# Kernel optimization log

Hardware: AMD Instinct MI355X
Metric: run time of the kernel (lower is better)

The kernel has to match this reference:

```python
import jax, jax.numpy as jnp
import numpy as np

HIDDEN = 4096
NUM_HEADS = 32
NUM_KV_HEADS = 8
HEAD_DIM = HIDDEN // NUM_HEADS  # 128
ROPE_THETA = 500000.0
WORLD_SIZE = 4  # number of ring blocks (simulated single-device)


def setup_inputs() -> dict:
    key = jax.random.key(0)
    ks = jax.random.split(key, 5)
    B, S = 1, 2048
    wscale = HIDDEN ** -0.5  # keep activations O(1)
    return {
        "hidden_states": jax.random.normal(ks[0], (B, S, HIDDEN), jnp.float32),
        "position_ids": jnp.broadcast_to(jnp.arange(S, dtype=jnp.int32), (B, S)),
        "q_proj": jax.random.normal(ks[1], (NUM_HEADS * HEAD_DIM, HIDDEN), jnp.float32) * wscale,
        "k_proj": jax.random.normal(ks[2], (NUM_KV_HEADS * HEAD_DIM, HIDDEN), jnp.float32) * wscale,
        "v_proj": jax.random.normal(ks[3], (NUM_KV_HEADS * HEAD_DIM, HIDDEN), jnp.float32) * wscale,
        "o_proj": jax.random.normal(ks[4], (HIDDEN, NUM_HEADS * HEAD_DIM), jnp.float32) * wscale,
    }


def _rope_cos_sin(position_ids):
    # LlamaRotaryEmbedding: inv_freq over even dims, emb = cat(freqs, freqs)
    inv_freq = 1.0 / (ROPE_THETA ** (jnp.arange(0, HEAD_DIM, 2, dtype=jnp.float32) / HEAD_DIM))
    freqs = position_ids.astype(jnp.float32)[..., None] * inv_freq  # [B,S,HD/2]
    emb = jnp.concatenate([freqs, freqs], axis=-1)                  # [B,S,HD]
    return jnp.cos(emb), jnp.sin(emb)


def _rotate_half(x):
    x1, x2 = jnp.split(x, 2, axis=-1)
    return jnp.concatenate([-x2, x1], axis=-1)


def _attention_forward(hidden_states, q_proj, k_proj, v_proj, o_proj, position_ids):
    B, S, _ = hidden_states.shape
    # projections (no bias), layout [B, S, H, D] as in the source (view before RoPE)
    q = (hidden_states @ q_proj.T).reshape(B, S, NUM_HEADS, HEAD_DIM)
    k = (hidden_states @ k_proj.T).reshape(B, S, NUM_KV_HEADS, HEAD_DIM)
    v = (hidden_states @ v_proj.T).reshape(B, S, NUM_KV_HEADS, HEAD_DIM)

    cos, sin = _rope_cos_sin(position_ids)        # [B,S,HD]
    c, s = cos[:, :, None, :], sin[:, :, None, :]  # unsqueeze_dim=2
    q = q * c + _rotate_half(q) * s
    k = k * c + _rotate_half(k) * s

    # GQA: expand KV heads to match query heads
    groups = NUM_HEADS // NUM_KV_HEADS
    k = jnp.repeat(k, groups, axis=2)  # [B,S,NH,HD]
    v = jnp.repeat(v, groups, axis=2)

    sm_scale = HEAD_DIM ** -0.5
    blk = S // WORLD_SIZE

    # ring: per-KV-block partial attention (non-causal, as no mask is passed) + LSE
    outs, lses = [], []
    for w in range(WORLD_SIZE):
        kb = k[:, w * blk:(w + 1) * blk]
        vb = v[:, w * blk:(w + 1) * blk]
        scores = jnp.einsum('bqhd,bkhd->bhqk', q, kb) * sm_scale  # [B,NH,S,blk]
        m = jnp.max(scores, axis=-1, keepdims=True)
        p = jnp.exp(scores - m)
        l = jnp.sum(p, axis=-1, keepdims=True)
        outs.append(jnp.einsum('bhqk,bkhd->bqhd', p / l, vb))      # normalized partial out
        lses.append((m + jnp.log(l))[..., 0])                      # [B,NH,S]

    # merge_attentions: weight each block by exp(lse_b - logsumexp(lse))
    lse_all = jnp.stack(lses, axis=0)                 # [W,B,NH,S]
    wgt = jax.nn.softmax(lse_all, axis=0)
    attn = sum(outs[w] * jnp.transpose(wgt[w], (0, 2, 1))[..., None]
               for w in range(WORLD_SIZE))            # [B,S,NH,HD]

    attn = attn.reshape(B, S, NUM_HEADS * HEAD_DIM)
    return attn @ o_proj.T


def reference(hidden_states, position_ids, q_proj, k_proj, v_proj, o_proj):
    return _attention_forward(hidden_states, q_proj, k_proj, v_proj, o_proj, position_ids)
```

## Files before the change

### kernel.cpp

```cpp
#include <hip/hip_runtime.h>
#include <stdint.h>
#include <cmath>

typedef unsigned short u16;
typedef unsigned int u32;
typedef __attribute__((ext_vector_type(8))) __bf16 bf16x8;
typedef __attribute__((ext_vector_type(4))) float f32x4;

#define HIDDEN 4096
#define NH 32
#define NKV 8
#define HD 128
#define S_LEN 2048

__device__ __forceinline__ u16 f2bf(float f) {
    u32 x = __float_as_uint(f);
    x += 0x7fff + ((x >> 16) & 1);
    return (u16)(x >> 16);
}
__device__ __forceinline__ float bf2f(u16 u) {
    return __uint_as_float(((u32)u) << 16);
}
__device__ __forceinline__ float fexp2(float x) {
#if __has_builtin(__builtin_amdgcn_exp2f)
    return __builtin_amdgcn_exp2f(x);
#else
    return __expf(x * 0.6931471805599453f);
#endif
}

template <int N>
__device__ __forceinline__ float dpp_ror(float v) {
    int i = __builtin_amdgcn_update_dpp(0, __float_as_int(v),
                                        0x120 + N, 0xf, 0xf, true);
    return __int_as_float(i);
}
__device__ __forceinline__ float row_max16(float x) {
    x = fmaxf(x, dpp_ror<1>(x));
    x = fmaxf(x, dpp_ror<2>(x));
    x = fmaxf(x, dpp_ror<4>(x));
    x = fmaxf(x, dpp_ror<8>(x));
    return x;
}
__device__ __forceinline__ float row_sum16(float x) {
    x += dpp_ror<1>(x);
    x += dpp_ror<2>(x);
    x += dpp_ror<4>(x);
    x += dpp_ror<8>(x);
    return x;
}

typedef __attribute__((address_space(1))) const void gv_t;
typedef __attribute__((address_space(3))) void lv_t;
__device__ __forceinline__ void async16(const u16* g, u16* s) {
    __builtin_amdgcn_global_load_lds((gv_t*)g, (lv_t*)s, 16, 0, 0);
}

#define F4_HS   2097152u
#define F4_WQ   4194304u
#define F4_WKV  1048576u
__global__ void cvt_all(const float* __restrict__ s0, const float* __restrict__ s1,
                        const float* __restrict__ s2, const float* __restrict__ s3,
                        const float* __restrict__ s4, u16* __restrict__ dst) {
    u32 i = blockIdx.x * 256 + threadIdx.x;
    const float* src; u32 off;
    if (i < F4_HS)                              { src = s0; off = 0; }
    else if (i < F4_HS + F4_WQ)                 { src = s1; off = F4_HS; }
    else if (i < F4_HS + F4_WQ + F4_WKV)        { src = s2; off = F4_HS + F4_WQ; }
    else if (i < F4_HS + F4_WQ + 2 * F4_WKV)    { src = s3; off = F4_HS + F4_WQ + F4_WKV; }
    else                                        { src = s4; off = F4_HS + F4_WQ + 2 * F4_WKV; }
    float4 v = ((const float4*)src)[i - off];
    union { u16 u[4]; uint2 w; } pk;
    pk.u[0] = f2bf(v.x); pk.u[1] = f2bf(v.y);
    pk.u[2] = f2bf(v.z); pk.u[3] = f2bf(v.w);
    ((uint2*)dst)[i] = pk.w;
}

#define GEMM_PROLOGUE_AND_MAINLOOP(Aptr, Bptr, Kdim)                                   \
    __shared__ u16 sA[128 * 64];                                                       \
    __shared__ u16 sB[128 * 64];                                                       \
    const int tid = threadIdx.x;                                                       \
    const int w = tid >> 6, lane = tid & 63;                                           \
    const int l15 = lane & 15, quad = lane >> 4;                                       \
    const int m0 = blockIdx.y * 128, n0 = blockIdx.x * 128;                            \
    const int wm = w & 1, wn = w >> 1;                                                 \
    f32x4 acc[4][4];                                                                   \
    _Pragma("unroll") for (int mi = 0; mi < 4; ++mi)                                   \
    _Pragma("unroll") for (int ni = 0; ni < 4; ++ni)                                   \
    _Pragma("unroll") for (int r = 0; r < 4; ++r) acc[mi][ni][r] = 0.f;                \
    for (int kt = 0; kt < (Kdim); kt += 64) {                                          \
        _Pragma("unroll") for (int i = 0; i < 4; ++i) {                                \
            int c = (i * 4 + w) * 64 + lane;                                           \
            int r = c >> 3, sl = c & 7, g = sl ^ (r & 7);                              \
            async16((Aptr) + (size_t)(m0 + r) * (Kdim) + kt + g * 8, &sA[c * 8]);      \
        }                                                                              \
        _Pragma("unroll") for (int i = 0; i < 4; ++i) {                                \
            int c = (i * 4 + w) * 64 + lane;                                           \
            int r = c >> 3, sl = c & 7, g = sl ^ (r & 7);                              \
            async16((Bptr) + (size_t)(n0 + r) * (Kdim) + kt + g * 8, &sB[c * 8]);      \
        }                                                                              \
        __syncthreads();                                                               \
        _Pragma("unroll") for (int ks = 0; ks < 2; ++ks) {                             \
            bf16x8 af[4], bf[4];                                                       \
            _Pragma("unroll") for (int t = 0; t < 4; ++t) {                            \
                int row = wm * 64 + t * 16 + l15;                                      \
                int sl = (ks * 4 + quad) ^ (row & 7);                                  \
                af[t] = *(const bf16x8*)&sA[row * 64 + sl * 8];                        \
            }                                                                          \
            _Pragma("unroll") for (int t = 0; t < 4; ++t) {                            \
                int row = wn * 64 + t * 16 + l15;                                      \
                int sl = (ks * 4 + quad) ^ (row & 7);                                  \
                bf[t] = *(const bf16x8*)&sB[row * 64 + sl * 8];                        \
            }                                                                          \
            _Pragma("unroll") for (int mi = 0; mi < 4; ++mi)                           \
            _Pragma("unroll") for (int ni = 0; ni < 4; ++ni)                           \
                acc[mi][ni] = __builtin_amdgcn_mfma_f32_16x16x32_bf16(                 \
                    af[mi], bf[ni], acc[mi][ni], 0, 0, 0);                             \
        }                                                                              \
        __syncthreads();                                                               \
    }

__global__ __launch_bounds__(256, 2) void gemm_bt_f32(
    const u16* __restrict__ A, const u16* __restrict__ B, float* __restrict__ C,
    int N, int K)
{
    GEMM_PROLOGUE_AND_MAINLOOP(A, B, K)
#pragma unroll
    for (int mi = 0; mi < 4; ++mi) {
        int row = m0 + wm * 64 + mi * 16 + quad * 4;
#pragma unroll
        for (int ni = 0; ni < 4; ++ni) {
            int col = n0 + wn * 64 + ni * 16 + l15;
#pragma unroll
            for (int r = 0; r < 4; ++r)
                C[(size_t)(row + r) * N + col] = acc[mi][ni][r];
        }
    }
}

__global__ __launch_bounds__(256, 2) void gemm_qkv(
    const u16* __restrict__ A, const u16* __restrict__ B,
    u16* __restrict__ qb, u16* __restrict__ kbuf, u16* __restrict__ vt)
{
    GEMM_PROLOGUE_AND_MAINLOOP(A, B, HIDDEN)
    if (n0 < 4096 + 1024) {
        u16* outp; int ldo, cb;
        if (n0 < 4096) { outp = qb; ldo = HIDDEN; cb = n0; }
        else           { outp = kbuf; ldo = NKV * HD; cb = n0 - 4096; }
#pragma unroll
        for (int mi = 0; mi < 4; ++mi) {
            int row = m0 + wm * 64 + mi * 16 + quad * 4;
#pragma unroll
            for (int ni = 0; ni < 4; ++ni) {
                int col = cb + wn * 64 + ni * 16 + l15;
#pragma unroll
                for (int r = 0; r < 4; ++r)
                    outp[(size_t)(row + r) * ldo + col] = f2bf(acc[mi][ni][r]);
            }
        }
    } else {
        int cb = n0 - (4096 + 1024);
#pragma unroll
        for (int mi = 0; mi < 4; ++mi) {
            int row = m0 + wm * 64 + mi * 16 + quad * 4;
#pragma unroll
            for (int ni = 0; ni < 4; ++ni) {
                int c = cb + wn * 64 + ni * 16 + l15;
                union { u16 u[4]; uint2 v; } pk;
#pragma unroll
                for (int r = 0; r < 4; ++r) pk.u[r] = f2bf(acc[mi][ni][r]);
                *(uint2*)&vt[(size_t)c * S_LEN + row] = pk.v;
            }
        }
    }
}

struct DTab { double f[64]; };
__global__ void rope_table(const int* __restrict__ pos, float2* __restrict__ tab,
                           DTab dt) {
    int idx = blockIdx.x * 256 + threadIdx.x;
    int d = idx & 63, s = idx >> 6;
    double fr = (double)pos[s] * dt.f[d];
    double sd, cd;
    sincos(fr, &sd, &cd);
    tab[idx] = make_float2((float)cd, (float)sd);
}

#define Q_ITEMS (S_LEN * NH * 64)
__global__ void rope_apply(u16* __restrict__ qb, u16* __restrict__ kb,
                           const float2* __restrict__ tab, float qscale) {
    int idx = blockIdx.x * 256 + threadIdx.x;
    u16* buf; int logH; float osc;
    if (idx < Q_ITEMS) { buf = qb; logH = 5; osc = qscale; }
    else { idx -= Q_ITEMS; buf = kb; logH = 3; osc = 1.0f; }
    int d = idx & 63;
    int rest = idx >> 6;
    int s = rest >> logH;
    float2 cs = tab[s * 64 + d];
    float c = cs.x * osc, sn = cs.y * osc;
    u16* p = buf + (size_t)rest * HD + d;
    float x1 = bf2f(p[0]), x2 = bf2f(p[64]);
    p[0]  = f2bf(x1 * c - x2 * sn);
    p[64] = f2bf(x2 * c + x1 * sn);
}

__global__ __launch_bounds__(256, 2) void attn_kernel(
    const u16* __restrict__ Q, const u16* __restrict__ Kb,
    const u16* __restrict__ Vt, u16* __restrict__ O)
{
    __shared__ u16 sK[64 * 128];
    __shared__ u16 sV[128 * 64];
    __shared__ __align__(16) u16 sP[4][8 * 264];
    __shared__ float sAl[4][32];

    const int tid = threadIdx.x;
    const int w = tid >> 6, lane = tid & 63;
    const int l15 = lane & 15, quad = lane >> 4;
    const int h = blockIdx.y, q0 = blockIdx.x * 128;
    const int hk = h >> 2;
    u16* const sPw = sP[w];

    bf16x8 qf[2][4];
#pragma unroll
    for (int mt = 0; mt < 2; ++mt)
#pragma unroll
        for (int ks = 0; ks < 4; ++ks)
            qf[mt][ks] = *(const bf16x8*)(Q + (size_t)(q0 + w * 32 + mt * 16 + l15) * HIDDEN
                                           + h * HD + ks * 32 + quad * 8);

    f32x4 oc[8][2];
#pragma unroll
    for (int dt = 0; dt < 8; ++dt)
#pragma unroll
        for (int nt = 0; nt < 2; ++nt)
#pragma unroll
            for (int r = 0; r < 4; ++r) oc[dt][nt][r] = 0.f;
    float m_r[2][4], l_r[2][4];
#pragma unroll
    for (int mt = 0; mt < 2; ++mt)
#pragma unroll
        for (int r = 0; r < 4; ++r) { m_r[mt][r] = -1e30f; l_r[mt][r] = 0.f; }

    auto stageK = [&](int k0) {
#pragma unroll
        for (int i = 0; i < 4; ++i) {
            int c = i * 256 + tid;
            int r = c >> 4, sl = c & 15, g = sl ^ (r & 15);
            async16(Kb + (size_t)(k0 + r) * (NKV * HD) + hk * HD + g * 8, &sK[c * 8]);
        }
    };
    auto stageV = [&](int k0) {
#pragma unroll
        for (int i = 0; i < 4; ++i) {
            int c = i * 256 + tid;
            int r = c >> 3, sl = c & 7, g = sl ^ (r & 7);
            async16(Vt + (size_t)(hk * HD + r) * S_LEN + k0 + g * 8, &sV[c * 8]);
        }
    };

    stageK(0);
    stageV(0);
    __syncthreads();

    for (int kbi = 0; kbi < 32; ++kbi) {
        f32x4 sa[2][4];
#pragma unroll
        for (int mt = 0; mt < 2; ++mt)
#pragma unroll
            for (int nt = 0; nt < 4; ++nt)
#pragma unroll
                for (int r = 0; r < 4; ++r) sa[mt][nt][r] = 0.f;
#pragma unroll
        for (int ks = 0; ks < 4; ++ks) {
            bf16x8 kf[4];
#pragma unroll
            for (int nt = 0; nt < 4; ++nt) {
                int row = nt * 16 + l15;
                int sl = (ks * 4 + quad) ^ (row & 15);
                kf[nt] = *(const bf16x8*)&sK[row * 128 + sl * 8];
            }
#pragma unroll
            for (int mt = 0; mt < 2; ++mt)
#pragma unroll
                for (int nt = 0; nt < 4; ++nt)
                    sa[mt][nt] = __builtin_amdgcn_mfma_f32_16x16x32_bf16(
                        qf[mt][ks], kf[nt], sa[mt][nt], 0, 0, 0);
        }

        float mxv[2][4];
        bool grow = false;
#pragma unroll
        for (int mt = 0; mt < 2; ++mt)
#pragma unroll
            for (int r = 0; r < 4; ++r) {
                float mx = sa[mt][0][r];
#pragma unroll
                for (int nt = 1; nt < 4; ++nt) mx = fmaxf(mx, sa[mt][nt][r]);
                mx = row_max16(mx);
                mxv[mt][r] = mx;
                grow = grow || (mx > m_r[mt][r] + 8.f);
            }
        const int dorescale = __any((int)grow);
        if (dorescale) {
#pragma unroll
            for (int mt = 0; mt < 2; ++mt)
#pragma unroll
                for (int r = 0; r < 4; ++r) {
                    float mnew = fmaxf(m_r[mt][r], mxv[mt][r]);
                    float alpha = fexp2(m_r[mt][r] - mnew);
                    m_r[mt][r] = mnew;
                    l_r[mt][r] *= alpha;
                    if (l15 == 0) sAl[w][mt * 16 + quad * 4 + r] = alpha;
                }
        }
#pragma unroll
        for (int mt = 0; mt < 2; ++mt)
#pragma unroll
            for (int r = 0; r < 4; ++r) {
                int ql = mt * 16 + quad * 4 + r;
                u16* pb = sPw + (l15 >> 3) * 264 + ql * 8 + (l15 & 7);
                float mm = m_r[mt][r];
                float rs = 0.f;
#pragma unroll
                for (int nt = 0; nt < 4; ++nt) {
                    float p = fexp2(sa[mt][nt][r] - mm);
                    rs += p;
                    pb[nt * 528] = f2bf(p);
                }
                rs = row_sum16(rs);
                l_r[mt][r] += rs;
            }

        __syncthreads();
        if (kbi < 31) stageK((kbi + 1) * 64);

        if (dorescale) {
            float al0 = sAl[w][l15], al1 = sAl[w][16 + l15];
#pragma unroll
            for (int dt = 0; dt < 8; ++dt)
#pragma unroll
                for (int r = 0; r < 4; ++r) { oc[dt][0][r] *= al0; oc[dt][1][r] *= al1; }
        }

#pragma unroll
        for (int ks = 0; ks < 2; ++ks) {
            bf16x8 vf[8], pf[2];
#pragma unroll
            for (int dt = 0; dt < 8; ++dt) {
                int row = dt * 16 + l15;
                int sl = (ks * 4 + quad) ^ (row & 7);
                vf[dt] = *(const bf16x8*)&sV[row * 64 + sl * 8];
            }
#pragma unroll
            for (int nt = 0; nt < 2; ++nt)
                pf[nt] = *(const bf16x8*)&sPw[(ks * 4 + quad) * 264 + (nt * 16 + l15) * 8];
#pragma unroll
            for (int dt = 0; dt < 8; ++dt)
#pragma unroll
                for (int nt = 0; nt < 2; ++nt)
                    oc[dt][nt] = __builtin_amdgcn_mfma_f32_16x16x32_bf16(
                        vf[dt], pf[nt], oc[dt][nt], 0, 0, 0);
        }

        __syncthreads();
        if (kbi < 31) stageV((kbi + 1) * 64);
    }

#pragma unroll
    for (int mt = 0; mt < 2; ++mt)
#pragma unroll
        for (int r = 0; r < 4; ++r)
            if (l15 == 0) sAl[w][mt * 16 + quad * 4 + r] = l_r[mt][r];
    float il[2];
    il[0] = 1.f / sAl[w][l15];
    il[1] = 1.f / sAl[w][16 + l15];
#pragma unroll
    for (int nt = 0; nt < 2; ++nt)
#pragma unroll
        for (int dt = 0; dt < 8; ++dt) {
            union { u16 u[4]; uint2 v; } pk;
#pragma unroll
            for (int r = 0; r < 4; ++r) pk.u[r] = f2bf(oc[dt][nt][r] * il[nt]);
            *(uint2*)(O + (size_t)(q0 + w * 32 + nt * 16 + l15) * HIDDEN
                        + h * HD + dt * 16 + quad * 4) = pk.v;
        }
}

extern "C" void kernel_launch(void* const* d_in, const int* in_sizes, int n_in,
                              void* d_out, int out_size, void* d_ws, size_t ws_size,
                              hipStream_t stream) {
    const float* hs = (const float*)d_in[0];
    const int* pos  = (const int*)d_in[1];
    const float* wq = (const float*)d_in[2];
    const float* wk = (const float*)d_in[3];
    const float* wv = (const float*)d_in[4];
    const float* wo = (const float*)d_in[5];
    float* out = (float*)d_out;

    u16* ws    = (u16*)d_ws;
    u16* hid16 = ws;
    u16* wq16  = hid16 + (size_t)S_LEN * HIDDEN;
    u16* wk16  = wq16 + (size_t)HIDDEN * HIDDEN;
    u16* wv16  = wk16 + (size_t)NKV * HD * HIDDEN;
    u16* wo16  = wv16 + (size_t)NKV * HD * HIDDEN;
    u16* qb    = wo16 + (size_t)HIDDEN * HIDDEN;
    u16* kb    = qb + (size_t)S_LEN * HIDDEN;
    u16* vt    = kb + (size_t)S_LEN * NKV * HD;
    u16* at    = vt + (size_t)S_LEN * NKV * HD;
    float2* tab = (float2*)(at + (size_t)S_LEN * HIDDEN);

    dim3 blk(256);

    cvt_all<<<dim3(12582912u / 256), blk, 0, stream>>>(hs, wq, wk, wv, wo, hid16);

    gemm_qkv<<<dim3((HIDDEN + 2 * NKV * HD) / 128, S_LEN / 128), blk, 0, stream>>>(
        hid16, wq16, qb, kb, vt);

    DTab dt;
    for (int i = 0; i < 64; ++i) dt.f[i] = pow(500000.0, -(double)i / 64.0);
    const float qscale = 0.08838834764831845f * 1.4426950408889634f;
    rope_table<<<dim3(S_LEN * 64 / 256), blk, 0, stream>>>(pos, tab, dt);
    rope_apply<<<dim3((Q_ITEMS + S_LEN * NKV * 64) / 256), blk, 0, stream>>>(
        qb, kb, tab, qscale);

    attn_kernel<<<dim3(S_LEN / 128, NH), dim3(256), 0, stream>>>(qb, kb, vt, at);

    gemm_bt_f32<<<dim3(HIDDEN / 128, S_LEN / 128), blk, 0, stream>>>(
        at, wo16, out, HIDDEN, HIDDEN);
}
```

Baseline: 487.9 us.

## Transpose QK^T MFMA to keep P in registers and double-buffer K/V

Computes S^T = K·Q^T so each lane holds scores for one query column, which lets the softmax probabilities feed the PV MFMA directly from registers. This removes the shared-memory P buffer, the alpha and l staging through LDS, and the DPP row reductions, replacing them with cross-quad shuffles. K and V tiles are now double-buffered, with the next tile prefetched at the top of each iteration, so only one barrier per iteration remains. Shared memory doubles to 64KB, which may limit occupancy to the requested 2 blocks per CU, and the V fragments are now read as split 8-byte loads.

```diff
diff --git a/kernel.cpp b/kernel.cpp
--- a/kernel.cpp
+++ b/kernel.cpp
@@ -27,27 +27,6 @@
 #else
     return __expf(x * 0.6931471805599453f);
 #endif
-}
-
-template <int N>
-__device__ __forceinline__ float dpp_ror(float v) {
-    int i = __builtin_amdgcn_update_dpp(0, __float_as_int(v),
-                                        0x120 + N, 0xf, 0xf, true);
-    return __int_as_float(i);
-}
-__device__ __forceinline__ float row_max16(float x) {
-    x = fmaxf(x, dpp_ror<1>(x));
-    x = fmaxf(x, dpp_ror<2>(x));
-    x = fmaxf(x, dpp_ror<4>(x));
-    x = fmaxf(x, dpp_ror<8>(x));
-    return x;
-}
-__device__ __forceinline__ float row_sum16(float x) {
-    x += dpp_ror<1>(x);
-    x += dpp_ror<2>(x);
-    x += dpp_ror<4>(x);
-    x += dpp_ror<8>(x);
-    return x;
 }
 
 typedef __attribute__((address_space(1))) const void gv_t;
@@ -208,17 +187,14 @@
     const u16* __restrict__ Q, const u16* __restrict__ Kb,
     const u16* __restrict__ Vt, u16* __restrict__ O)
 {
-    __shared__ u16 sK[64 * 128];
-    __shared__ u16 sV[128 * 64];
-    __shared__ __align__(16) u16 sP[4][8 * 264];
-    __shared__ float sAl[4][32];
+    __shared__ u16 sK[2][64 * 128];
+    __shared__ u16 sV[2][128 * 64];
 
     const int tid = threadIdx.x;
     const int w = tid >> 6, lane = tid & 63;
     const int l15 = lane & 15, quad = lane >> 4;
     const int h = blockIdx.y, q0 = blockIdx.x * 128;
     const int hk = h >> 2;
-    u16* const sPw = sP[w];
 
     bf16x8 qf[2][4];
 #pragma unroll
@@ -235,41 +211,47 @@
         for (int nt = 0; nt < 2; ++nt)
 #pragma unroll
             for (int r = 0; r < 4; ++r) oc[dt][nt][r] = 0.f;
-    float m_r[2][4], l_r[2][4];
-#pragma unroll
-    for (int mt = 0; mt < 2; ++mt)
-#pragma unroll
-        for (int r = 0; r < 4; ++r) { m_r[mt][r] = -1e30f; l_r[mt][r] = 0.f; }
-
-    auto stageK = [&](int k0) {
+    float m_r[2], l_r[2];
+#pragma unroll
+    for (int mt = 0; mt < 2; ++mt) { m_r[mt] = -1e30f; l_r[mt] = 0.f; }
+
+    auto stageK = [&](int k0, u16* dst) {
 #pragma unroll
         for (int i = 0; i < 4; ++i) {
             int c = i * 256 + tid;
             int r = c >> 4, sl = c & 15, g = sl ^ (r & 15);
-            async16(Kb + (size_t)(k0 + r) * (NKV * HD) + hk * HD + g * 8, &sK[c * 8]);
+            async16(Kb + (size_t)(k0 + r) * (NKV * HD) + hk * HD + g * 8, &dst[c * 8]);
         }
     };
-    auto stageV = [&](int k0) {
+    auto stageV = [&](int k0, u16* dst) {
 #pragma unroll
         for (int i = 0; i < 4; ++i) {
             int c = i * 256 + tid;
             int r = c >> 3, sl = c & 7, g = sl ^ (r & 7);
-            async16(Vt + (size_t)(hk * HD + r) * S_LEN + k0 + g * 8, &sV[c * 8]);
+            async16(Vt + (size_t)(hk * HD + r) * S_LEN + k0 + g * 8, &dst[c * 8]);
         }
     };
 
-    stageK(0);
-    stageV(0);
+    stageK(0, sK[0]);
+    stageV(0, sV[0]);
     __syncthreads();
 
+    int cur = 0;
     for (int kbi = 0; kbi < 32; ++kbi) {
-        f32x4 sa[2][4];
-#pragma unroll
-        for (int mt = 0; mt < 2; ++mt)
-#pragma unroll
-            for (int nt = 0; nt < 4; ++nt)
-#pragma unroll
-                for (int r = 0; r < 4; ++r) sa[mt][nt][r] = 0.f;
+        if (kbi < 31) {
+            stageK((kbi + 1) * 64, sK[cur ^ 1]);
+            stageV((kbi + 1) * 64, sV[cur ^ 1]);
+        }
+        const u16* sKc = sK[cur];
+        const u16* sVc = sV[cur];
+
+        f32x4 sa[4][2];
+#pragma unroll
+        for (int nt = 0; nt < 4; ++nt)
+#pragma unroll
+            for (int mt = 0; mt < 2; ++mt)
+#pragma unroll
+                for (int r = 0; r < 4; ++r) sa[nt][mt][r] = 0.f;
 #pragma unroll
         for (int ks = 0; ks < 4; ++ks) {
             bf16x8 kf[4];
@@ -277,103 +259,97 @@
             for (int nt = 0; nt < 4; ++nt) {
                 int row = nt * 16 + l15;
                 int sl = (ks * 4 + quad) ^ (row & 15);
-                kf[nt] = *(const bf16x8*)&sK[row * 128 + sl * 8];
-            }
-#pragma unroll
-            for (int mt = 0; mt < 2; ++mt)
-#pragma unroll
-                for (int nt = 0; nt < 4; ++nt)
-                    sa[mt][nt] = __builtin_amdgcn_mfma_f32_16x16x32_bf16(
-                        qf[mt][ks], kf[nt], sa[mt][nt], 0, 0, 0);
-        }
-
-        float mxv[2][4];
+                kf[nt] = *(const bf16x8*)&sKc[row * 128 + sl * 8];
+            }
+#pragma unroll
+            for (int nt = 0; nt < 4; ++nt)
+#pragma unroll
+                for (int mt = 0; mt < 2; ++mt)
+                    sa[nt][mt] = __builtin_amdgcn_mfma_f32_16x16x32_bf16(
+                        kf[nt], qf[mt][ks], sa[nt][mt], 0, 0, 0);
+        }
+
+        float mxv[2];
         bool grow = false;
 #pragma unroll
-        for (int mt = 0; mt < 2; ++mt)
-#pragma unroll
-            for (int r = 0; r < 4; ++r) {
-                float mx = sa[mt][0][r];
-#pragma unroll
-                for (int nt = 1; nt < 4; ++nt) mx = fmaxf(mx, sa[mt][nt][r]);
-                mx = row_max16(mx);
-                mxv[mt][r] = mx;
-                grow = grow || (mx > m_r[mt][r] + 8.f);
-            }
+        for (int mt = 0; mt < 2; ++mt) {
+            float mx = sa[0][mt][0];
+#pragma unroll
+            for (int nt = 0; nt < 4; ++nt)
+#pragma unroll
+                for (int r = 0; r < 4; ++r)
+                    if (nt || r) mx = fmaxf(mx, sa[nt][mt][r]);
+            mx = fmaxf(mx, __shfl_xor(mx, 16));
+            mx = fmaxf(mx, __shfl_xor(mx, 32));
+            mxv[mt] = mx;
+            grow = grow || (mx > m_r[mt] + 8.f);
+        }
         const int dorescale = __any((int)grow);
         if (dorescale) {
-#pragma unroll
-            for (int mt = 0; mt < 2; ++mt)
-#pragma unroll
-                for (int r = 0; r < 4; ++r) {
-                    float mnew = fmaxf(m_r[mt][r], mxv[mt][r]);
-                    float alpha = fexp2(m_r[mt][r] - mnew);
-                    m_r[mt][r] = mnew;
-                    l_r[mt][r] *= alpha;
-                    if (l15 == 0) sAl[w][mt * 16 + quad * 4 + r] = alpha;
-                }
-        }
-#pragma unroll
-        for (int mt = 0; mt < 2; ++mt)
-#pragma unroll
-            for (int r = 0; r < 4; ++r) {
-                int ql = mt * 16 + quad * 4 + r;
-                u16* pb = sPw + (l15 >> 3) * 264 + ql * 8 + (l15 & 7);
-                float mm = m_r[mt][r];
-                float rs = 0.f;
-#pragma unroll
-                for (int nt = 0; nt < 4; ++nt) {
-                    float p = fexp2(sa[mt][nt][r] - mm);
-                    rs += p;
-                    pb[nt * 528] = f2bf(p);
-                }
-                rs = row_sum16(rs);
-                l_r[mt][r] += rs;
-            }
-
-        __syncthreads();
-        if (kbi < 31) stageK((kbi + 1) * 64);
-
-        if (dorescale) {
-            float al0 = sAl[w][l15], al1 = sAl[w][16 + l15];
+            float al[2];
+#pragma unroll
+            for (int mt = 0; mt < 2; ++mt) {
+                float mnew = fmaxf(m_r[mt], mxv[mt]);
+                al[mt] = fexp2(m_r[mt] - mnew);
+                m_r[mt] = mnew;
+                l_r[mt] *= al[mt];
+            }
 #pragma unroll
             for (int dt = 0; dt < 8; ++dt)
 #pragma unroll
-                for (int r = 0; r < 4; ++r) { oc[dt][0][r] *= al0; oc[dt][1][r] *= al1; }
+                for (int r = 0; r < 4; ++r) { oc[dt][0][r] *= al[0]; oc[dt][1][r] *= al[1]; }
+        }
+
+        bf16x8 pf[2][2];
+#pragma unroll
+        for (int mt = 0; mt < 2; ++mt) {
+            float mm = m_r[mt];
+            float lsum = 0.f;
+#pragma unroll
+            for (int ntk = 0; ntk < 4; ++ntk) {
+                float p0 = fexp2(sa[ntk][mt][0] - mm);
+                float p1 = fexp2(sa[ntk][mt][1] - mm);
+                float p2 = fexp2(sa[ntk][mt][2] - mm);
+                float p3 = fexp2(sa[ntk][mt][3] - mm);
+                lsum += (p0 + p1) + (p2 + p3);
+                const int kx = ntk >> 1, e = (ntk & 1) * 4;
+                pf[kx][mt][e + 0] = (__bf16)p0;
+                pf[kx][mt][e + 1] = (__bf16)p1;
+                pf[kx][mt][e + 2] = (__bf16)p2;
+                pf[kx][mt][e + 3] = (__bf16)p3;
+            }
+            l_r[mt] += lsum;
         }
 
 #pragma unroll
         for (int ks = 0; ks < 2; ++ks) {
-            bf16x8 vf[8], pf[2];
 #pragma unroll
             for (int dt = 0; dt < 8; ++dt) {
                 int row = dt * 16 + l15;
-                int sl = (ks * 4 + quad) ^ (row & 7);
-                vf[dt] = *(const bf16x8*)&sV[row * 64 + sl * 8];
-            }
-#pragma unroll
-            for (int nt = 0; nt < 2; ++nt)
-                pf[nt] = *(const bf16x8*)&sPw[(ks * 4 + quad) * 264 + (nt * 16 + l15) * 8];
-#pragma unroll
-            for (int dt = 0; dt < 8; ++dt)
+                int g1 = (ks * 4 + (quad >> 1)) ^ (row & 7);
+                int base = row * 64 + (quad & 1) * 4;
+                union { uint2 u2[2]; bf16x8 v; } vfu;
+                vfu.u2[0] = *(const uint2*)&sVc[base + g1 * 8];
+                vfu.u2[1] = *(const uint2*)&sVc[base + (g1 ^ 2) * 8];
 #pragma unroll
                 for (int nt = 0; nt < 2; ++nt)
                     oc[dt][nt] = __builtin_amdgcn_mfma_f32_16x16x32_bf16(
-                        vf[dt], pf[nt], oc[dt][nt], 0, 0, 0);
+                        vfu.v, pf[ks][nt], oc[dt][nt], 0, 0, 0);
+            }
         }
 
         __syncthreads();
-        if (kbi < 31) stageV((kbi + 1) * 64);
+        cur ^= 1;
     }
 
-#pragma unroll
-    for (int mt = 0; mt < 2; ++mt)
-#pragma unroll
-        for (int r = 0; r < 4; ++r)
-            if (l15 == 0) sAl[w][mt * 16 + quad * 4 + r] = l_r[mt][r];
     float il[2];
-    il[0] = 1.f / sAl[w][l15];
-    il[1] = 1.f / sAl[w][16 + l15];
+#pragma unroll
+    for (int mt = 0; mt < 2; ++mt) {
+        float ls = l_r[mt];
+        ls += __shfl_xor(ls, 16);
+        ls += __shfl_xor(ls, 32);
+        il[mt] = 1.f / ls;
+    }
 #pragma unroll
     for (int nt = 0; nt < 2; ++nt)
 #pragma unroll
```

After: 465.7 us. -4.5%, faster.
